# Optimization experiments

Hardware: AMD Instinct MI355X
Metric: run time of the kernel (lower is better)

## Reference

```python
import jax, jax.numpy as jnp
import numpy as np

N, E, F_IN, HID, HEADS, OUT, NGRAPH = 50000, 800000, 128, 64, 4, 64, 512
NEG_SLOPE = 0.2


def setup_inputs() -> dict:
    key = jax.random.key(0)
    ks = jax.random.split(key, 16)
    d1 = HID * HEADS  # 256
    inp = {
        "x": jax.random.normal(ks[0], (N, F_IN), jnp.float32),
        "edge_index": jax.random.randint(ks[1], (2, E), 0, N, jnp.int64),
        "batch": jnp.sort(jax.random.randint(ks[2], (N,), 0, NGRAPH, jnp.int64)),
        # layer 1 params (GATConv(F_IN -> HID, heads=HEADS, concat=True))
        "W1": jax.random.normal(ks[3], (F_IN, d1), jnp.float32) * 0.05,
        "att_src1": jax.random.normal(ks[4], (HEADS, HID), jnp.float32) * 0.05,
        "att_dst1": jax.random.normal(ks[5], (HEADS, HID), jnp.float32) * 0.05,
        "b1": jnp.zeros((d1,), jnp.float32),
        # layer 2 params (GATConv(d1 -> HID, heads=HEADS, concat=True))
        "W2": jax.random.normal(ks[6], (d1, d1), jnp.float32) * 0.05,
        "att_src2": jax.random.normal(ks[7], (HEADS, HID), jnp.float32) * 0.05,
        "att_dst2": jax.random.normal(ks[8], (HEADS, HID), jnp.float32) * 0.05,
        "b2": jnp.zeros((d1,), jnp.float32),
        # final linear
        "fc_w": jax.random.normal(ks[9], (d1, OUT), jnp.float32) * 0.05,
        "fc_b": jnp.zeros((OUT,), jnp.float32),
    }
    return inp


def _gat_layer(x, src, dst, W, att_src, att_dst, bias):
    # linear transform, split into heads: [N, H, C]
    h = (x @ W).reshape(N, HEADS, HID)
    # per-node attention logits (a^T h), per head: [N, H]
    a_s = jnp.einsum("nhc,hc->nh", h, att_src)
    a_d = jnp.einsum("nhc,hc->nh", h, att_dst)
    # per-edge logits with leaky relu: [E', H]
    e = a_s[src] + a_d[dst]
    e = jnp.where(e > 0, e, NEG_SLOPE * e)
    # segment softmax over edges grouped by destination node
    m = jax.ops.segment_max(e, dst, num_segments=N)
    ex = jnp.exp(e - m[dst])
    s = jax.ops.segment_sum(ex, dst, num_segments=N)
    alpha = ex / s[dst]  # every node has a self-loop -> s > 0
    # weighted message aggregation: scatter-add of alpha * h_src
    out = jax.ops.segment_sum(h[src] * alpha[:, :, None], dst, num_segments=N)
    return out.reshape(N, HEADS * HID) + bias


def reference(x, edge_index, batch, W1, att_src1, att_dst1, b1,
              W2, att_src2, att_dst2, b2, fc_w, fc_b):
    # PyG GATConv default add_self_loops=True
    loop = jnp.arange(N, dtype=edge_index.dtype)
    src = jnp.concatenate([edge_index[0], loop])
    dst = jnp.concatenate([edge_index[1], loop])

    h = _gat_layer(x, src, dst, W1, att_src1, att_dst1, b1)
    h = jax.nn.elu(h)  # dropout is identity in eval mode
    h = _gat_layer(h, src, dst, W2, att_src2, att_dst2, b2)
    h = jax.nn.elu(h)

    # global mean pool over graphs
    sums = jax.ops.segment_sum(h, batch, num_segments=NGRAPH)
    cnts = jax.ops.segment_sum(jnp.ones((N,), h.dtype), batch, num_segments=NGRAPH)
    pooled = sums / jnp.maximum(cnts, 1.0)[:, None]

    return pooled @ fc_w + fc_b
```

## Files before the change

### kernel.cpp

```cpp
#include <hip/hip_runtime.h>
#include <cstddef>
#include <cstdint>

#define NN 50000
#define EE 800000
#define FIN 128
#define D1 256
#define HID 64
#define HEADS 4
#define NG 512
#define FOUT 64
#define NEG_SLOPE 0.2f
#define CAP 96

typedef _Float16 f16x8 __attribute__((ext_vector_type(8)));
typedef _Float16 f16x4 __attribute__((ext_vector_type(4)));
typedef float f32x4 __attribute__((ext_vector_type(4)));

__device__ __forceinline__ float leaky(float x) { return x > 0.f ? x : NEG_SLOPE * x; }

__global__ void k_scatter_direct(const int* __restrict__ ei, int* __restrict__ cnt,
                                 int* __restrict__ slot) {
    int i = blockIdx.x * 256 + threadIdx.x;
    if (i < EE) {
        int s = ei[i], d = ei[EE + i];
        int p = atomicAdd(&cnt[d], 1);
        if (p < CAP)
            __builtin_nontemporal_store(s, &slot[(size_t)d * CAP + p]);
    }
}

#define XB ((NN * FIN / 8 + 255) / 256)
#define WB ((256 * (FIN + D1) + 255) / 256)
#define CB ((NN + 255) / 256)

__global__ void k_cvt_all(const float* __restrict__ x, const float* __restrict__ W1,
                          const float* __restrict__ W2, _Float16* __restrict__ x16,
                          _Float16* __restrict__ w1t, _Float16* __restrict__ w2t,
                          int* __restrict__ cnt) {
    int bid = blockIdx.x;
    if (bid < XB) {
        int i = bid * 256 + threadIdx.x;
        if (bid < CB) {
            int ci = bid * 256 + threadIdx.x;
            if (ci < NN) cnt[ci] = 0;
        }
        if (i < NN * FIN / 8) {
            const float4 v0 = *(const float4*)(x + (size_t)i * 8);
            const float4 v1 = *(const float4*)(x + (size_t)i * 8 + 4);
            f16x8 o;
            o[0] = (_Float16)v0.x; o[1] = (_Float16)v0.y;
            o[2] = (_Float16)v0.z; o[3] = (_Float16)v0.w;
            o[4] = (_Float16)v1.x; o[5] = (_Float16)v1.y;
            o[6] = (_Float16)v1.z; o[7] = (_Float16)v1.w;
            *(f16x8*)(x16 + (size_t)i * 8) = o;
        }
    } else {
        int idx = (bid - XB) * 256 + threadIdx.x;
        if (idx < 256 * FIN) {
            int n = idx / FIN, k = idx - n * FIN;
            w1t[idx] = (_Float16)W1[(size_t)k * 256 + n];
        } else if (idx < 256 * FIN + 256 * D1) {
            int j = idx - 256 * FIN;
            int n = j >> 8, k = j & 255;
            w2t[j] = (_Float16)W2[(size_t)k * 256 + n];
        }
    }
}

#define BM 128
#define BN 128
#define BK 64
#define LDK (BK + 4)

template <int K>
__global__ __launch_bounds__(256) void k_gemm(const _Float16* __restrict__ A,
                                              const _Float16* __restrict__ Bt,
                                              _Float16* __restrict__ C,
                                              const float* __restrict__ att_s,
                                              const float* __restrict__ att_d,
                                              float* __restrict__ a_s,
                                              float* __restrict__ a_d) {
    __shared__ _Float16 As[BM][LDK];
    const int tid = threadIdx.x;
    const int lane = tid & 63;
    const int wave = tid >> 6;
    const int wm = wave & 1, wn = wave >> 1;
    const int m0 = blockIdx.x * BM;
    const int n0 = blockIdx.y * BN;
    const int row_m = lane & 15, quad = lane >> 4;

    f32x4 acc[4][4];
#pragma unroll
    for (int mi = 0; mi < 4; ++mi)
#pragma unroll
        for (int ni = 0; ni < 4; ++ni)
#pragma unroll
            for (int r = 0; r < 4; ++r) acc[mi][ni][r] = 0.f;

    const int c8 = (tid & 7) * 8;
    const int rr = tid >> 3;
    const _Float16* bp = Bt + (size_t)(n0 + wn * 64 + row_m) * K + quad * 8;

    for (int k0 = 0; k0 < K; k0 += BK) {
#pragma unroll
        for (int p = 0; p < 4; ++p) {
            int r = p * 32 + rr;
            int gr = m0 + r; gr = gr < NN ? gr : NN - 1;
            f16x8 v = *(const f16x8*)(A + (size_t)gr * K + k0 + c8);
            *(f16x8*)(&As[r][c8]) = v;
        }
        __syncthreads();
#pragma unroll
        for (int kc = 0; kc < BK; kc += 32) {
            f16x8 af[4], bf[4];
#pragma unroll
            for (int mi = 0; mi < 4; ++mi)
                af[mi] = *(const f16x8*)(&As[wm * 64 + mi * 16 + row_m][kc + quad * 8]);
#pragma unroll
            for (int ni = 0; ni < 4; ++ni)
                bf[ni] = *(const f16x8*)(bp + (size_t)ni * 16 * K + k0 + kc);
#pragma unroll
            for (int mi = 0; mi < 4; ++mi)
#pragma unroll
                for (int ni = 0; ni < 4; ++ni)
                    acc[mi][ni] = __builtin_amdgcn_mfma_f32_16x16x32_f16(
                        bf[ni], af[mi], acc[mi][ni], 0, 0, 0);
        }
        __syncthreads();
    }
#pragma unroll
    for (int mi = 0; mi < 4; ++mi) {
        int m = m0 + wm * 64 + mi * 16 + row_m;
        if (m < NN) {
#pragma unroll
            for (int ni = 0; ni < 4; ++ni) {
                f16x4 o;
                o[0] = (_Float16)acc[mi][ni][0];
                o[1] = (_Float16)acc[mi][ni][1];
                o[2] = (_Float16)acc[mi][ni][2];
                o[3] = (_Float16)acc[mi][ni][3];
                *(f16x4*)(C + (size_t)m * D1 + n0 + wn * 64 + ni * 16 + quad * 4) = o;
            }
        }
    }
    const int head = blockIdx.y * 2 + wn;
    const float* attsv = att_s + head * HID;
    const float* attdv = att_d + head * HID;
    float avs[4][4], avd[4][4];
#pragma unroll
    for (int ni = 0; ni < 4; ++ni)
#pragma unroll
        for (int r = 0; r < 4; ++r) {
            avs[ni][r] = attsv[ni * 16 + quad * 4 + r];
            avd[ni][r] = attdv[ni * 16 + quad * 4 + r];
        }
#pragma unroll
    for (int mi = 0; mi < 4; ++mi) {
        float ps = 0.f, pd = 0.f;
#pragma unroll
        for (int ni = 0; ni < 4; ++ni)
#pragma unroll
            for (int r = 0; r < 4; ++r) {
                ps += acc[mi][ni][r] * avs[ni][r];
                pd += acc[mi][ni][r] * avd[ni][r];
            }
        ps += __shfl_xor(ps, 16); ps += __shfl_xor(ps, 32);
        pd += __shfl_xor(pd, 16); pd += __shfl_xor(pd, 32);
        int m = m0 + wm * 64 + mi * 16 + row_m;
        if (quad == 0 && m < NN) {
            a_s[m * 4 + head] = ps;
            a_d[m * 4 + head] = pd;
        }
    }
}

__global__ __launch_bounds__(64) void k_aggregate(
    const _Float16* __restrict__ h, const float* __restrict__ a_s,
    const float* __restrict__ a_d, const int* __restrict__ cnt,
    const int* __restrict__ slot, const float* __restrict__ bias,
    _Float16* __restrict__ out, int apply_elu) {
    const int n = blockIdx.x;
    const int tid = threadIdx.x;
    const int myhead = tid >> 4;
    const int c4 = tid * 4;
    const int start = n * CAP;
    const int deg = cnt[n];
    const int end = start + (deg < CAP ? deg : CAP);

    __shared__ float s_w[64][4];

    const float4 ad = *(const float4*)(a_d + (size_t)n * 4);

    const float4 asn = *(const float4*)(a_s + (size_t)n * 4);
    float w0 = __expf(leaky(asn.x + ad.x));
    float w1 = __expf(leaky(asn.y + ad.y));
    float w2 = __expf(leaky(asn.z + ad.z));
    float w3 = __expf(leaky(asn.w + ad.w));
    const float wself = (myhead == 0) ? w0 : (myhead == 1) ? w1 : (myhead == 2) ? w2 : w3;
    const f16x4 hn = *(const f16x4*)(h + ((size_t)n << 8) + c4);
    float l = wself;
    float4 acc = make_float4(wself * (float)hn[0], wself * (float)hn[1],
                             wself * (float)hn[2], wself * (float)hn[3]);

    for (int base = start; base < end; base += 64) {
        const int len = min(64, end - base);
        if (tid < len) {
            const int s = slot[base + tid];
            const float4 as = *(const float4*)(a_s + (size_t)s * 4);
            s_w[tid][0] = __expf(leaky(as.x + ad.x));
            s_w[tid][1] = __expf(leaky(as.y + ad.y));
            s_w[tid][2] = __expf(leaky(as.z + ad.z));
            s_w[tid][3] = __expf(leaky(as.w + ad.w));
        }
        __syncthreads();
#pragma unroll 4
        for (int jj = 0; jj < len; ++jj) {
            const int s = slot[base + jj];
            const float w = s_w[jj][myhead];
            const f16x4 hv = *(const f16x4*)(h + ((size_t)s << 8) + c4);
            l += w;
            acc.x += w * (float)hv[0];
            acc.y += w * (float)hv[1];
            acc.z += w * (float)hv[2];
            acc.w += w * (float)hv[3];
        }
        __syncthreads();
    }
    const float inv = 1.f / l;
    const float4 bb = *(const float4*)(bias + c4);
    float vx = acc.x * inv + bb.x;
    float vy = acc.y * inv + bb.y;
    float vz = acc.z * inv + bb.z;
    float vw = acc.w * inv + bb.w;
    if (apply_elu) {
        vx = vx > 0.f ? vx : expm1f(vx);
        vy = vy > 0.f ? vy : expm1f(vy);
        vz = vz > 0.f ? vz : expm1f(vz);
        vw = vw > 0.f ? vw : expm1f(vw);
    }
    f16x4 o;
    o[0] = (_Float16)vx; o[1] = (_Float16)vy; o[2] = (_Float16)vz; o[3] = (_Float16)vw;
    *(f16x4*)(out + (size_t)n * D1 + c4) = o;
}

__global__ __launch_bounds__(256) void k_pool_fc(const _Float16* __restrict__ h,
                                                 const int* __restrict__ batch,
                                                 const float* __restrict__ fc_w,
                                                 const float* __restrict__ fc_b,
                                                 float* __restrict__ out) {
    __shared__ float row[D1];
    int g = blockIdx.x, c = threadIdx.x;
    int lo = 0, hi = NN;
    while (lo < hi) { int mid = (lo + hi) >> 1; if (batch[mid] < g) lo = mid + 1; else hi = mid; }
    int start = lo;
    hi = NN;
    while (lo < hi) { int mid = (lo + hi) >> 1; if (batch[mid] < g + 1) lo = mid + 1; else hi = mid; }
    int end = lo;

    float acc = 0.f;
    for (int n = start; n < end; ++n) acc += (float)h[(size_t)n * D1 + c];
    float inv = 1.f / fmaxf((float)(end - start), 1.f);
    row[c] = acc * inv;
    __syncthreads();
    if (c < FOUT) {
        float o = 0.f;
#pragma unroll 4
        for (int k = 0; k < D1; ++k) o += row[k] * fc_w[k * FOUT + c];
        out[(size_t)g * FOUT + c] = o + fc_b[c];
    }
}

extern "C" void kernel_launch(void* const* d_in, const int* in_sizes, int n_in,
                              void* d_out, int out_size, void* d_ws, size_t ws_size,
                              hipStream_t stream) {
    const float* x        = (const float*)d_in[0];
    const int*   ei       = (const int*)d_in[1];
    const int*   batch    = (const int*)d_in[2];
    const float* W1       = (const float*)d_in[3];
    const float* att_src1 = (const float*)d_in[4];
    const float* att_dst1 = (const float*)d_in[5];
    const float* b1       = (const float*)d_in[6];
    const float* W2       = (const float*)d_in[7];
    const float* att_src2 = (const float*)d_in[8];
    const float* att_dst2 = (const float*)d_in[9];
    const float* b2       = (const float*)d_in[10];
    const float* fc_w     = (const float*)d_in[11];
    const float* fc_b     = (const float*)d_in[12];
    float* out = (float*)d_out;

    _Float16* h_pre  = (_Float16*)d_ws;
    _Float16* h_act  = h_pre + (size_t)NN * D1;
    _Float16* x16    = h_act + (size_t)NN * D1;
    _Float16* w1t    = x16 + (size_t)NN * FIN;
    _Float16* w2t    = w1t + 256 * FIN;
    float* a_s       = (float*)(w2t + 256 * D1);
    float* a_d       = a_s + (size_t)NN * 4;
    int*   cnt       = (int*)(a_d + (size_t)NN * 4);
    int*   slot      = cnt + NN;

    const int nblk_edges = (EE + 255) / 256;

    k_cvt_all<<<XB + WB, 256, 0, stream>>>(x, W1, W2, x16, w1t, w2t, cnt);
    k_scatter_direct<<<nblk_edges, 256, 0, stream>>>(ei, cnt, slot);

    dim3 ggrid((NN + BM - 1) / BM, D1 / BN);

    k_gemm<FIN><<<ggrid, 256, 0, stream>>>(x16, w1t, h_pre,
                                           att_src1, att_dst1, a_s, a_d);
    k_aggregate<<<NN, 64, 0, stream>>>(h_pre, a_s, a_d, cnt, slot, b1, h_act, 1);

    k_gemm<D1><<<ggrid, 256, 0, stream>>>(h_act, w2t, h_pre,
                                          att_src2, att_dst2, a_s, a_d);
    k_aggregate<<<NN, 64, 0, stream>>>(h_pre, a_s, a_d, cnt, slot, b2, h_act, 1);

    k_pool_fc<<<NG, 256, 0, stream>>>(h_act, batch, fc_w, fc_b, out);
}
```

Measured before the change: 377.9 us.

## Fuse edge scatter into layer-1 GEMM launch and stage B tile in LDS

Merges the edge bucketing scatter kernel into the first GEMM launch as extra blocks, so the independent scatter and GEMM work share one grid and can overlap, and one launch is removed. The GEMM body also now stages the transposed weight tile in shared memory instead of reading B fragments directly from global memory per wave. This uses more LDS per block, which may lower occupancy, and adds block-index dispatch in the fused kernel.

```diff
diff --git a/kernel.cpp b/kernel.cpp
--- a/kernel.cpp
+++ b/kernel.cpp
@@ -19,17 +19,6 @@
 
 __device__ __forceinline__ float leaky(float x) { return x > 0.f ? x : NEG_SLOPE * x; }
 
-__global__ void k_scatter_direct(const int* __restrict__ ei, int* __restrict__ cnt,
-                                 int* __restrict__ slot) {
-    int i = blockIdx.x * 256 + threadIdx.x;
-    if (i < EE) {
-        int s = ei[i], d = ei[EE + i];
-        int p = atomicAdd(&cnt[d], 1);
-        if (p < CAP)
-            __builtin_nontemporal_store(s, &slot[(size_t)d * CAP + p]);
-    }
-}
-
 #define XB ((NN * FIN / 8 + 255) / 256)
 #define WB ((256 * (FIN + D1) + 255) / 256)
 #define CB ((NN + 255) / 256)
@@ -74,20 +63,19 @@
 #define LDK (BK + 4)
 
 template <int K>
-__global__ __launch_bounds__(256) void k_gemm(const _Float16* __restrict__ A,
-                                              const _Float16* __restrict__ Bt,
-                                              _Float16* __restrict__ C,
-                                              const float* __restrict__ att_s,
-                                              const float* __restrict__ att_d,
-                                              float* __restrict__ a_s,
-                                              float* __restrict__ a_d) {
+__device__ __forceinline__ void gemm_logits_body(
+    const _Float16* __restrict__ A, const _Float16* __restrict__ Bt,
+    _Float16* __restrict__ C, const float* __restrict__ att_s,
+    const float* __restrict__ att_d, float* __restrict__ a_s,
+    float* __restrict__ a_d, int bx, int by) {
     __shared__ _Float16 As[BM][LDK];
+    __shared__ _Float16 Bs[BN][LDK];
     const int tid = threadIdx.x;
     const int lane = tid & 63;
     const int wave = tid >> 6;
     const int wm = wave & 1, wn = wave >> 1;
-    const int m0 = blockIdx.x * BM;
-    const int n0 = blockIdx.y * BN;
+    const int m0 = bx * BM;
+    const int n0 = by * BN;
     const int row_m = lane & 15, quad = lane >> 4;
 
     f32x4 acc[4][4];
@@ -100,7 +88,6 @@
 
     const int c8 = (tid & 7) * 8;
     const int rr = tid >> 3;
-    const _Float16* bp = Bt + (size_t)(n0 + wn * 64 + row_m) * K + quad * 8;
 
     for (int k0 = 0; k0 < K; k0 += BK) {
 #pragma unroll
@@ -110,6 +97,12 @@
             f16x8 v = *(const f16x8*)(A + (size_t)gr * K + k0 + c8);
             *(f16x8*)(&As[r][c8]) = v;
         }
+#pragma unroll
+        for (int p = 0; p < 4; ++p) {
+            int r = p * 32 + rr;
+            f16x8 v = *(const f16x8*)(Bt + (size_t)(n0 + r) * K + k0 + c8);
+            *(f16x8*)(&Bs[r][c8]) = v;
+        }
         __syncthreads();
 #pragma unroll
         for (int kc = 0; kc < BK; kc += 32) {
@@ -119,7 +112,7 @@
                 af[mi] = *(const f16x8*)(&As[wm * 64 + mi * 16 + row_m][kc + quad * 8]);
 #pragma unroll
             for (int ni = 0; ni < 4; ++ni)
-                bf[ni] = *(const f16x8*)(bp + (size_t)ni * 16 * K + k0 + kc);
+                bf[ni] = *(const f16x8*)(&Bs[wn * 64 + ni * 16 + row_m][kc + quad * 8]);
 #pragma unroll
             for (int mi = 0; mi < 4; ++mi)
 #pragma unroll
@@ -144,7 +137,7 @@
             }
         }
     }
-    const int head = blockIdx.y * 2 + wn;
+    const int head = by * 2 + wn;
     const float* attsv = att_s + head * HID;
     const float* attdv = att_d + head * HID;
     float avs[4][4], avd[4][4];
@@ -173,6 +166,38 @@
             a_d[m * 4 + head] = pd;
         }
     }
+}
+
+#define GB1 (((NN + BM - 1) / BM) * 2)
+#define SB ((EE + 255) / 256)
+
+__global__ __launch_bounds__(256) void k_gemm1_scatter(
+    const _Float16* __restrict__ x16, const _Float16* __restrict__ w1t,
+    _Float16* __restrict__ C, const float* __restrict__ att_s,
+    const float* __restrict__ att_d, float* __restrict__ a_s,
+    float* __restrict__ a_d, const int* __restrict__ ei,
+    int* __restrict__ cnt, int* __restrict__ slot) {
+    if (blockIdx.x < GB1) {
+        gemm_logits_body<FIN>(x16, w1t, C, att_s, att_d, a_s, a_d,
+                              blockIdx.x >> 1, blockIdx.x & 1);
+    } else {
+        int i = (blockIdx.x - GB1) * 256 + threadIdx.x;
+        if (i < EE) {
+            int s = ei[i], d = ei[EE + i];
+            int p = atomicAdd(&cnt[d], 1);
+            if (p < CAP)
+                __builtin_nontemporal_store(s, &slot[(size_t)d * CAP + p]);
+        }
+    }
+}
+
+__global__ __launch_bounds__(256) void k_gemm2(
+    const _Float16* __restrict__ A, const _Float16* __restrict__ Bt,
+    _Float16* __restrict__ C, const float* __restrict__ att_s,
+    const float* __restrict__ att_d, float* __restrict__ a_s,
+    float* __restrict__ a_d) {
+    gemm_logits_body<D1>(A, Bt, C, att_s, att_d, a_s, a_d,
+                         blockIdx.x, blockIdx.y);
 }
 
 __global__ __launch_bounds__(64) void k_aggregate(
@@ -299,19 +324,17 @@
     int*   cnt       = (int*)(a_d + (size_t)NN * 4);
     int*   slot      = cnt + NN;
 
-    const int nblk_edges = (EE + 255) / 256;
-
     k_cvt_all<<<XB + WB, 256, 0, stream>>>(x, W1, W2, x16, w1t, w2t, cnt);
-    k_scatter_direct<<<nblk_edges, 256, 0, stream>>>(ei, cnt, slot);
+
+    k_gemm1_scatter<<<GB1 + SB, 256, 0, stream>>>(x16, w1t, h_pre,
+                                                  att_src1, att_dst1, a_s, a_d,
+                                                  ei, cnt, slot);
+
+    k_aggregate<<<NN, 64, 0, stream>>>(h_pre, a_s, a_d, cnt, slot, b1, h_act, 1);
 
     dim3 ggrid((NN + BM - 1) / BM, D1 / BN);
-
-    k_gemm<FIN><<<ggrid, 256, 0, stream>>>(x16, w1t, h_pre,
-                                           att_src1, att_dst1, a_s, a_d);
-    k_aggregate<<<NN, 64, 0, stream>>>(h_pre, a_s, a_d, cnt, slot, b1, h_act, 1);
-
-    k_gemm<D1><<<ggrid, 256, 0, stream>>>(h_act, w2t, h_pre,
-                                          att_src2, att_dst2, a_s, a_d);
+    k_gemm2<<<ggrid, 256, 0, stream>>>(h_act, w2t, h_pre,
+                                       att_src2, att_dst2, a_s, a_d);
     k_aggregate<<<NN, 64, 0, stream>>>(h_pre, a_s, a_d, cnt, slot, b2, h_act, 1);
 
     k_pool_fc<<<NG, 256, 0, stream>>>(h_act, batch, fc_w, fc_b, out);
```

New measurement: 363.4 us. 3.8% less time.
